# Kernel optimization log

Hardware: AMD Instinct MI355X
Metric: run time of the kernel (lower is better)

The kernel has to match this reference:

```python
import jax, jax.numpy as jnp
import numpy as np

NUM_CLASSES = 43
IMG_SIZE = 640.0
ALPHA, GAMMA = 0.25, 2.0
EPS = 1e-07


def _focal_loss(pred, target):
    p = jnp.clip(pred, EPS, 1.0 - EPS)
    pos = (target > 0.5).astype(p.dtype)
    neg = (target <= 0.5).astype(p.dtype)
    pos_loss = -ALPHA * (1.0 - p) ** GAMMA * jnp.log(p) * pos * target
    neg_loss = -(1.0 - ALPHA) * p ** GAMMA * jnp.log(1.0 - p) * neg * (1.0 - target)
    num_pos = jnp.maximum(pos.sum(), 1.0)
    return (pos_loss + neg_loss).sum() / num_pos


def _generate_targets(bboxes, labels, h, w):
    # bboxes: [B, M, 4] x1y1x2y2 in pixels; labels: [B, M] int (-1 = pad)
    B, M = labels.shape
    stride = IMG_SIZE / h
    x1, y1, x2, y2 = [bboxes[..., i] for i in range(4)]
    cx, cy = (x1 + x2) / 2.0, (y1 + y2) / 2.0
    bw, bh = x2 - x1, y2 - y1
    valid = (labels >= 0) & (bboxes.sum(-1) > 0) & (bw > 0) & (bh > 0)  # [B, M]

    gx = jnp.clip((cx / stride).astype(jnp.int32), 0, w - 1)
    gy = jnp.clip((cy / stride).astype(jnp.int32), 0, h - 1)
    # radius = sqrt(bw*bh)/stride clamped to >=2, then truncated to int
    r = jnp.maximum(jnp.sqrt(bw * bh) / stride, 2.0).astype(jnp.int32).astype(jnp.float32)
    sigma = r / 2.0

    gxf = gx.astype(jnp.float32)[:, :, None, None]  # [B,M,1,1]
    gyf = gy.astype(jnp.float32)[:, :, None, None]
    xg = jnp.arange(w, dtype=jnp.float32)[None, None, None, :]
    yg = jnp.arange(h, dtype=jnp.float32)[None, None, :, None]
    dist_sq = (xg - gxf) ** 2 + (yg - gyf) ** 2  # [B,M,H,W]
    r4 = r[:, :, None, None]
    s4 = sigma[:, :, None, None]
    gauss = jnp.exp(-dist_sq / (2.0 * s4 * s4))
    gauss = gauss * (dist_sq <= (2.0 * r4) ** 2) * valid[:, :, None, None]
    heatmap = gauss.max(axis=1)[:, None]  # [B,1,H,W]; max with implicit 0 init (gauss>=0)

    grid_cx = (gx.astype(jnp.float32) + 0.5) * stride
    grid_cy = (gy.astype(jnp.float32) + 0.5) * stride
    dx = (cx - grid_cx) / stride
    dy = (cy - grid_cy) / stride
    dw = jnp.log(bw / stride + 1e-06)
    dh = jnp.log(bh / stride + 1e-06)

    b_idx = jnp.broadcast_to(jnp.arange(B)[:, None], (B, M))
    gy_s = jnp.where(valid, gy, h)  # out-of-bounds -> dropped
    lab_s = jnp.clip(labels, 0, NUM_CLASSES - 1)

    box_targets = jnp.zeros((B, 4, h, w), jnp.float32)
    box_targets = box_targets.at[b_idx, 0, gy_s, gx].set(dx, mode='drop')
    box_targets = box_targets.at[b_idx, 1, gy_s, gx].set(dy, mode='drop')
    box_targets = box_targets.at[b_idx, 2, gy_s, gx].set(dw, mode='drop')
    box_targets = box_targets.at[b_idx, 3, gy_s, gx].set(dh, mode='drop')
    class_targets = jnp.zeros((B, NUM_CLASSES, h, w), jnp.float32)
    class_targets = class_targets.at[b_idx, lab_s, gy_s, gx].set(1.0, mode='drop')
    mask = jnp.zeros((B, 1, h, w), jnp.float32)
    mask = mask.at[b_idx, 0, gy_s, gx].set(1.0, mode='drop')
    return heatmap, box_targets, class_targets, mask


def setup_inputs() -> dict:
    key = jax.random.key(0)
    k1, k2, k3, k4, k5, k6 = jax.random.split(key, 6)
    B, M, H, W = 16, 64, 160, 160
    pred_heatmap = jax.random.uniform(k1, (B, 1, H, W), jnp.float32)
    pred_boxes = jax.random.normal(k2, (B, 4, H, W), jnp.float32)
    pred_classes = jax.random.normal(k3, (B, NUM_CLASSES, H, W), jnp.float32)
    pts = jax.random.uniform(k4, (B, M, 2, 2), jnp.float32) * IMG_SIZE  # two corners
    lo = jnp.min(pts, axis=2)
    hi = jnp.max(pts, axis=2) + 1.0
    bboxes = jnp.concatenate([lo, hi], axis=-1)  # x1,y1,x2,y2
    labels = jax.random.randint(k5, (B, M), 0, NUM_CLASSES)
    drop = jax.random.uniform(k6, (B, M)) < 0.3
    labels = jnp.where(drop, -1, labels).astype(jnp.int64)
    return {"pred_heatmap": pred_heatmap, "pred_boxes": pred_boxes,
            "pred_classes": pred_classes, "bboxes": bboxes, "labels": labels}


def reference(pred_heatmap, pred_boxes, pred_classes, bboxes, labels):
    B, _, h, w = pred_heatmap.shape
    t_heat, t_box, t_cls, mask = _generate_targets(bboxes, labels, h, w)
    heat_loss = _focal_loss(pred_heatmap, t_heat)
    num_pos = jnp.maximum(mask.sum(), 1.0)
    l1 = jnp.abs(pred_boxes * mask - t_box * mask).sum()
    box_loss = jnp.where(num_pos > 1, l1 / num_pos, 0.0)
    cmask = jnp.broadcast_to(mask, t_cls.shape)
    cls_raw = _focal_loss(jax.nn.sigmoid(pred_classes) * cmask, t_cls * cmask)
    cls_loss = jnp.where(num_pos > 1, cls_raw, 0.0)
    total = heat_loss + box_loss + cls_loss  # lambdas all 1.0
    return total
```

## Files before the change

### kernel.cpp

```cpp
#include <hip/hip_runtime.h>

#define HH 160
#define WW 160
#define HW (HH*WW)
#define NB 16
#define NM 64
#define NC 43
#define BLKX 25
#define NHEAT (NB*BLKX)
#define NCELL (NB*16)

constexpr float STRIDE = 4.0f;
constexpr float EPSF = 1e-7f;
constexpr float BIGF = 3.4e38f;

__device__ __forceinline__ void box_geom4(const float4* __restrict__ bb4,
                                          const int* __restrict__ labels, int t,
                                          bool& valid, int& gx, int& gy,
                                          float& cx, float& cy, float& bw, float& bh) {
  float4 v = bb4[t];
  cx = (v.x + v.z) * 0.5f;
  cy = (v.y + v.w) * 0.5f;
  bw = v.z - v.x;
  bh = v.w - v.y;
  int lab = labels[t];
  valid = (lab >= 0) && ((v.x + v.y + v.z + v.w) > 0.0f) && (bw > 0.0f) && (bh > 0.0f);
  int tgx = (int)(cx * 0.25f);
  int tgy = (int)(cy * 0.25f);
  gx = tgx < 0 ? 0 : (tgx > WW - 1 ? WW - 1 : tgx);
  gy = tgy < 0 ? 0 : (tgy > HH - 1 ? HH - 1 : tgy);
}

__global__ __launch_bounds__(256) void k_fused(const float* __restrict__ pred_heat,
                                               const float* __restrict__ pred_boxes,
                                               const float* __restrict__ pred_classes,
                                               const float4* __restrict__ bboxes,
                                               const int* __restrict__ labels,
                                               float2* __restrict__ heatp,
                                               float4* __restrict__ cellsp) {
  __shared__ float4 sp[NM];
  __shared__ float lred[4];
  __shared__ int nred[4];
  __shared__ float4 cred[4];

  int b = blockIdx.y, bx = blockIdx.x;
  int tid = threadIdx.x;
  int wave = tid >> 6, lane = tid & 63;

  int pixbase = bx * 1024 + tid * 4;
  int idx = b * HW + pixbase;
  float4 pr4 = *(const float4*)(pred_heat + idx);

  bool cellsblk = (bx < 16);
  bool iswin = false;
  float xcls = 0.0f, pbv = 0.0f;
  unsigned long long cm = 0;
  float cx_m, cy_m, bw_m, bh_m;
  int gx_m, gy_m;
  if (cellsblk) {
    int m = bx * 4 + wave;
    int lbox = b * NM + lane;
    bool valid; int gx, gy; float cx, cy, bw, bh;
    box_geom4(bboxes, labels, lbox, valid, gx, gy, cx, cy, bw, bh);
    int lab = labels[lbox]; lab = lab < 0 ? 0 : (lab > NC - 1 ? NC - 1 : lab);

    int valid_m = __shfl((int)valid, m);
    gx_m = __shfl(gx, m); gy_m = __shfl(gy, m);
    cx_m = __shfl(cx, m); cy_m = __shfl(cy, m);
    bw_m = __shfl(bw, m); bh_m = __shfl(bh, m);

    if (valid_m) {
      bool maps = valid && (gx == gx_m) && (gy == gy_m);
      unsigned long long mk = __ballot(maps);
      if ((63 - __clzll(mk)) == m) {
        iswin = true;
        cm = maps ? (1ull << lab) : 0ull;
        #pragma unroll
        for (int o = 1; o < 64; o <<= 1) cm |= __shfl_xor(cm, o);
        int celloff = gy_m * WW + gx_m;
        if (lane < NC)
          xcls = pred_classes[(size_t)b * NC * HW + (size_t)lane * HW + celloff];
        else if (lane < NC + 4)
          pbv = pred_boxes[(size_t)b * 4 * HW + (size_t)(lane - NC) * HW + celloff];
      }
    }
  }

  if (tid < NM) {
    int t = b * NM + tid;
    bool valid; int gx, gy; float cx, cy, bw, bh;
    box_geom4(bboxes, labels, t, valid, gx, gy, cx, cy, bw, bh);
    float rf = fmaxf(sqrtf(bw * bh) * 0.25f, 2.0f);
    float r = (float)(int)rf;
    float z = 2.0f / (r * r);
    float gxf = (float)gx, gyf = (float)gy;
    float4 p;
    p.x = z;
    p.y = -2.0f * z * gxf;
    p.z = -2.0f * z * gyf;
    p.w = valid ? z * fmaf(gxf, gxf, gyf * gyf) : __int_as_float(0x7fc00000);
    sp[tid] = p;
  }
  __syncthreads();

  int row = pixbase / WW;
  float xf0 = (float)(pixbase - row * WW);
  float yf = (float)row;
  float xf1 = xf0 + 1.0f, xf2 = xf0 + 2.0f, xf3 = xf0 + 3.0f;
  float yy = yf * yf;
  float s0 = fmaf(xf0, xf0, yy), s1 = fmaf(xf1, xf1, yy);
  float s2 = fmaf(xf2, xf2, yy), s3 = fmaf(xf3, xf3, yy);

  float m0 = BIGF, m1 = BIGF, m2 = BIGF, m3 = BIGF;
  #pragma unroll
  for (int m = 0; m < NM; m += 2) {
    float4 c0 = sp[m], c1 = sp[m + 1];
    { float base = fmaf(c0.z, yf, c0.w);
      m0 = fminf(m0, fmaf(c0.x, s0, fmaf(c0.y, xf0, base)));
      m1 = fminf(m1, fmaf(c0.x, s1, fmaf(c0.y, xf1, base)));
      m2 = fminf(m2, fmaf(c0.x, s2, fmaf(c0.y, xf2, base)));
      m3 = fminf(m3, fmaf(c0.x, s3, fmaf(c0.y, xf3, base))); }
    { float base = fmaf(c1.z, yf, c1.w);
      m0 = fminf(m0, fmaf(c1.x, s0, fmaf(c1.y, xf0, base)));
      m1 = fminf(m1, fmaf(c1.x, s1, fmaf(c1.y, xf1, base)));
      m2 = fminf(m2, fmaf(c1.x, s2, fmaf(c1.y, xf2, base)));
      m3 = fminf(m3, fmaf(c1.x, s3, fmaf(c1.y, xf3, base))); }
  }

  float t0 = (m0 <= 8.0f) ? __expf(-m0) : 0.0f;
  float t1 = (m1 <= 8.0f) ? __expf(-m1) : 0.0f;
  float t2 = (m2 <= 8.0f) ? __expf(-m2) : 0.0f;
  float t3 = (m3 <= 8.0f) ? __expf(-m3) : 0.0f;
  float p0 = fminf(fmaxf(pr4.x, EPSF), 1.0f - EPSF);
  float p1 = fminf(fmaxf(pr4.y, EPSF), 1.0f - EPSF);
  float p2 = fminf(fmaxf(pr4.z, EPSF), 1.0f - EPSF);
  float p3 = fminf(fmaxf(pr4.w, EPSF), 1.0f - EPSF);
  float q0 = 1.0f - p0, q1 = 1.0f - p1, q2 = 1.0f - p2, q3 = 1.0f - p3;
  bool o0 = t0 > 0.5f, o1 = t1 > 0.5f, o2 = t2 > 0.5f, o3 = t3 > 0.5f;
  float lg0 = __logf(o0 ? p0 : q0), lg1 = __logf(o1 ? p1 : q1);
  float lg2 = __logf(o2 ? p2 : q2), lg3 = __logf(o3 ? p3 : q3);
  float cf0 = o0 ? (-0.25f * q0 * q0 * t0) : (-0.75f * p0 * p0 * (1.0f - t0));
  float cf1 = o1 ? (-0.25f * q1 * q1 * t1) : (-0.75f * p1 * p1 * (1.0f - t1));
  float cf2 = o2 ? (-0.25f * q2 * q2 * t2) : (-0.75f * p2 * p2 * (1.0f - t2));
  float cf3 = o3 ? (-0.25f * q3 * q3 * t3) : (-0.75f * p3 * p3 * (1.0f - t3));
  float loss = fmaf(cf0, lg0, cf1 * lg1) + fmaf(cf2, lg2, cf3 * lg3);

  int cnt = __popcll(__ballot(o0)) + __popcll(__ballot(o1)) +
            __popcll(__ballot(o2)) + __popcll(__ballot(o3));
  #pragma unroll
  for (int off = 32; off > 0; off >>= 1) loss += __shfl_down(loss, off);
  if (lane == 0) { lred[wave] = loss; nred[wave] = cnt; }
  __syncthreads();
  if (tid == 0)
    heatp[b * BLKX + bx] = make_float2(lred[0] + lred[1] + lred[2] + lred[3],
                                       (float)(nred[0] + nred[1] + nred[2] + nred[3]));

  if (cellsblk) {
    float l1 = 0.0f, csum = 0.0f, cnt1 = 0.0f, npos = 0.0f;
    if (iswin) {
      if (lane < NC) {
        float s = 1.0f / (1.0f + __expf(-xcls));
        float pc = fminf(fmaxf(s, EPSF), 1.0f - EPSF);
        float omc = 1.0f - pc;
        csum = ((cm >> lane) & 1ull) ? (-0.25f * omc * omc * __logf(pc))
                                     : (-0.75f * pc * pc * __logf(omc));
      }
      float dxv = (cx_m - ((float)gx_m + 0.5f) * STRIDE) * 0.25f;
      float dyv = (cy_m - ((float)gy_m + 0.5f) * STRIDE) * 0.25f;
      int li = lane - NC;
      float tlin = (li == 0) ? dxv : dyv;
      float tlog = __logf(((li == 2) ? bw_m : bh_m) * 0.25f + 1e-6f);
      float targ = (li < 2) ? tlin : tlog;
      float l1c = (li >= 0 && li < 4) ? fabsf(pbv - targ) : 0.0f;
      #pragma unroll
      for (int o = 32; o > 0; o >>= 1) {
        csum += __shfl_down(csum, o);
        l1c  += __shfl_down(l1c, o);
      }
      l1 = l1c;
      cnt1 = (lane == 0) ? 1.0f : 0.0f;
      npos = (float)__popcll(cm);
    }
    if (lane == 0) cred[wave] = make_float4(l1, cnt1, csum, npos);
    __syncthreads();
    if (tid == 0) {
      float4 a = cred[0], c1 = cred[1], c2 = cred[2], c3 = cred[3];
      cellsp[b * 16 + bx] = make_float4(a.x + c1.x + c2.x + c3.x,
                                        a.y + c1.y + c2.y + c3.y,
                                        a.z + c1.z + c2.z + c3.z,
                                        a.w + c1.w + c2.w + c3.w);
    }
  }
}

__global__ __launch_bounds__(512) void k_final(const float2* __restrict__ heatp,
                                               const float4* __restrict__ cellsp,
                                               float* __restrict__ out) {
  int t = threadIdx.x;
  double hs = 0.0, hc = 0.0, l1 = 0.0, mc = 0.0, cs = 0.0, cp = 0.0;
  if (t < NHEAT) {
    float2 v = heatp[t];
    hs = (double)v.x; hc = (double)v.y;
  }
  if (t < NCELL) {
    float4 e = cellsp[t];
    l1 = (double)e.x; mc = (double)e.y; cs = (double)e.z; cp = (double)e.w;
  }
  #pragma unroll
  for (int off = 32; off > 0; off >>= 1) {
    hs += __shfl_down(hs, off); hc += __shfl_down(hc, off);
    l1 += __shfl_down(l1, off); mc += __shfl_down(mc, off);
    cs += __shfl_down(cs, off); cp += __shfl_down(cp, off);
  }
  __shared__ double fin[8][6];
  int wave = t >> 6;
  if ((t & 63) == 0) {
    fin[wave][0] = hs; fin[wave][1] = hc; fin[wave][2] = l1;
    fin[wave][3] = mc; fin[wave][4] = cs; fin[wave][5] = cp;
  }
  __syncthreads();
  if (t == 0) {
    double HS = 0, HC = 0, L1 = 0, MC = 0, CS = 0, CP = 0;
    #pragma unroll
    for (int i = 0; i < 8; ++i) {
      HS += fin[i][0]; HC += fin[i][1]; L1 += fin[i][2];
      MC += fin[i][3]; CS += fin[i][4]; CP += fin[i][5];
    }
    double nph = HC < 1.0 ? 1.0 : HC;
    float heat = (float)(HS / nph);
    float box = 0.0f, cls = 0.0f;
    if (MC > 1.5) {
      box = (float)(L1 / MC);
      double c = CP < 1.0 ? 1.0 : CP;
      cls = (float)(CS / c);
    }
    out[0] = heat + box + cls;
  }
}

extern "C" void kernel_launch(void* const* d_in, const int* in_sizes, int n_in,
                              void* d_out, int out_size, void* d_ws, size_t ws_size,
                              hipStream_t stream) {
  const float*  pred_heat    = (const float*)d_in[0];
  const float*  pred_boxes   = (const float*)d_in[1];
  const float*  pred_classes = (const float*)d_in[2];
  const float4* bboxes       = (const float4*)d_in[3];
  const int*    labels       = (const int*)d_in[4];

  char* ws = (char*)d_ws;
  float2* heatp  = (float2*)ws;
  float4* cellsp = (float4*)(ws + 3200);

  dim3 grid(BLKX, NB);
  k_fused<<<grid, 256, 0, stream>>>(pred_heat, pred_boxes, pred_classes,
                                    bboxes, labels, heatp, cellsp);
  k_final<<<1, 512, 0, stream>>>(heatp, cellsp, (float*)d_out);
}
```

Baseline: 14.45 us.

## Split heatmap and per-cell work into separate block groups

The per-box cell work (class focal loss and box L1 at winning cells) now runs in 16 extra blocks per batch instead of sharing blocks with the heatmap computation. This is meant to shorten the critical path of the first 16 blocks, which previously did both jobs serially, and to spread the gathers across more CUs. The cost is 256 more blocks in the grid, each with its own launch and reduction overhead.

After: 14.43 us. No clear change (-0.1%).

```diff
diff --git a/kernel.cpp b/kernel.cpp
--- a/kernel.cpp
+++ b/kernel.cpp
@@ -47,145 +47,138 @@
   int tid = threadIdx.x;
   int wave = tid >> 6, lane = tid & 63;
 
-  int pixbase = bx * 1024 + tid * 4;
-  int idx = b * HW + pixbase;
-  float4 pr4 = *(const float4*)(pred_heat + idx);
-
-  bool cellsblk = (bx < 16);
-  bool iswin = false;
-  float xcls = 0.0f, pbv = 0.0f;
-  unsigned long long cm = 0;
-  float cx_m, cy_m, bw_m, bh_m;
-  int gx_m, gy_m;
-  if (cellsblk) {
-    int m = bx * 4 + wave;
+  if (bx < BLKX) {
+    int pixbase = bx * 1024 + tid * 4;
+    int idx = b * HW + pixbase;
+    float4 pr4 = *(const float4*)(pred_heat + idx);
+
+    if (tid < NM) {
+      int t = b * NM + tid;
+      bool valid; int gx, gy; float cx, cy, bw, bh;
+      box_geom4(bboxes, labels, t, valid, gx, gy, cx, cy, bw, bh);
+      float rf = fmaxf(sqrtf(bw * bh) * 0.25f, 2.0f);
+      float r = (float)(int)rf;
+      float z = 2.0f / (r * r);
+      float gxf = (float)gx, gyf = (float)gy;
+      float4 p;
+      p.x = z;
+      p.y = -2.0f * z * gxf;
+      p.z = -2.0f * z * gyf;
+      p.w = valid ? z * fmaf(gxf, gxf, gyf * gyf) : __int_as_float(0x7fc00000);
+      sp[tid] = p;
+    }
+    __syncthreads();
+
+    int row = pixbase / WW;
+    float xf0 = (float)(pixbase - row * WW);
+    float yf = (float)row;
+    float xf1 = xf0 + 1.0f, xf2 = xf0 + 2.0f, xf3 = xf0 + 3.0f;
+    float yy = yf * yf;
+    float s0 = fmaf(xf0, xf0, yy), s1 = fmaf(xf1, xf1, yy);
+    float s2 = fmaf(xf2, xf2, yy), s3 = fmaf(xf3, xf3, yy);
+
+    float m0 = BIGF, m1 = BIGF, m2 = BIGF, m3 = BIGF;
+    #pragma unroll
+    for (int m = 0; m < NM; m += 2) {
+      float4 c0 = sp[m], c1 = sp[m + 1];
+      { float base = fmaf(c0.z, yf, c0.w);
+        m0 = fminf(m0, fmaf(c0.x, s0, fmaf(c0.y, xf0, base)));
+        m1 = fminf(m1, fmaf(c0.x, s1, fmaf(c0.y, xf1, base)));
+        m2 = fminf(m2, fmaf(c0.x, s2, fmaf(c0.y, xf2, base)));
+        m3 = fminf(m3, fmaf(c0.x, s3, fmaf(c0.y, xf3, base))); }
+      { float base = fmaf(c1.z, yf, c1.w);
+        m0 = fminf(m0, fmaf(c1.x, s0, fmaf(c1.y, xf0, base)));
+        m1 = fminf(m1, fmaf(c1.x, s1, fmaf(c1.y, xf1, base)));
+        m2 = fminf(m2, fmaf(c1.x, s2, fmaf(c1.y, xf2, base)));
+        m3 = fminf(m3, fmaf(c1.x, s3, fmaf(c1.y, xf3, base))); }
+    }
+
+    float t0 = (m0 <= 8.0f) ? __expf(-m0) : 0.0f;
+    float t1 = (m1 <= 8.0f) ? __expf(-m1) : 0.0f;
+    float t2 = (m2 <= 8.0f) ? __expf(-m2) : 0.0f;
+    float t3 = (m3 <= 8.0f) ? __expf(-m3) : 0.0f;
+    float p0 = fminf(fmaxf(pr4.x, EPSF), 1.0f - EPSF);
+    float p1 = fminf(fmaxf(pr4.y, EPSF), 1.0f - EPSF);
+    float p2 = fminf(fmaxf(pr4.z, EPSF), 1.0f - EPSF);
+    float p3 = fminf(fmaxf(pr4.w, EPSF), 1.0f - EPSF);
+    float q0 = 1.0f - p0, q1 = 1.0f - p1, q2 = 1.0f - p2, q3 = 1.0f - p3;
+    bool o0 = t0 > 0.5f, o1 = t1 > 0.5f, o2 = t2 > 0.5f, o3 = t3 > 0.5f;
+    float lg0 = __logf(o0 ? p0 : q0), lg1 = __logf(o1 ? p1 : q1);
+    float lg2 = __logf(o2 ? p2 : q2), lg3 = __logf(o3 ? p3 : q3);
+    float cf0 = o0 ? (-0.25f * q0 * q0 * t0) : (-0.75f * p0 * p0 * (1.0f - t0));
+    float cf1 = o1 ? (-0.25f * q1 * q1 * t1) : (-0.75f * p1 * p1 * (1.0f - t1));
+    float cf2 = o2 ? (-0.25f * q2 * q2 * t2) : (-0.75f * p2 * p2 * (1.0f - t2));
+    float cf3 = o3 ? (-0.25f * q3 * q3 * t3) : (-0.75f * p3 * p3 * (1.0f - t3));
+    float loss = fmaf(cf0, lg0, cf1 * lg1) + fmaf(cf2, lg2, cf3 * lg3);
+
+    int cnt = __popcll(__ballot(o0)) + __popcll(__ballot(o1)) +
+              __popcll(__ballot(o2)) + __popcll(__ballot(o3));
+    #pragma unroll
+    for (int off = 32; off > 0; off >>= 1) loss += __shfl_down(loss, off);
+    if (lane == 0) { lred[wave] = loss; nred[wave] = cnt; }
+    __syncthreads();
+    if (tid == 0)
+      heatp[b * BLKX + bx] =
+          make_float2(lred[0] + lred[1] + lred[2] + lred[3],
+                      (float)(nred[0] + nred[1] + nred[2] + nred[3]));
+  } else {
+    int cb = bx - BLKX;
+    int m = cb * 4 + wave;
     int lbox = b * NM + lane;
     bool valid; int gx, gy; float cx, cy, bw, bh;
     box_geom4(bboxes, labels, lbox, valid, gx, gy, cx, cy, bw, bh);
     int lab = labels[lbox]; lab = lab < 0 ? 0 : (lab > NC - 1 ? NC - 1 : lab);
 
-    int valid_m = __shfl((int)valid, m);
-    gx_m = __shfl(gx, m); gy_m = __shfl(gy, m);
-    cx_m = __shfl(cx, m); cy_m = __shfl(cy, m);
-    bw_m = __shfl(bw, m); bh_m = __shfl(bh, m);
-
+    int   valid_m = __shfl((int)valid, m);
+    int   gx_m = __shfl(gx, m), gy_m = __shfl(gy, m);
+    float cx_m = __shfl(cx, m), cy_m = __shfl(cy, m);
+    float bw_m = __shfl(bw, m), bh_m = __shfl(bh, m);
+
+    float l1 = 0.0f, csum = 0.0f, cnt1 = 0.0f, npos = 0.0f;
     if (valid_m) {
       bool maps = valid && (gx == gx_m) && (gy == gy_m);
       unsigned long long mk = __ballot(maps);
       if ((63 - __clzll(mk)) == m) {
-        iswin = true;
-        cm = maps ? (1ull << lab) : 0ull;
+        unsigned long long cm = maps ? (1ull << lab) : 0ull;
         #pragma unroll
         for (int o = 1; o < 64; o <<= 1) cm |= __shfl_xor(cm, o);
         int celloff = gy_m * WW + gx_m;
+
+        float xcls = 0.0f, pbv = 0.0f;
         if (lane < NC)
           xcls = pred_classes[(size_t)b * NC * HW + (size_t)lane * HW + celloff];
         else if (lane < NC + 4)
           pbv = pred_boxes[(size_t)b * 4 * HW + (size_t)(lane - NC) * HW + celloff];
+
+        if (lane < NC) {
+          float s = 1.0f / (1.0f + __expf(-xcls));
+          float pc = fminf(fmaxf(s, EPSF), 1.0f - EPSF);
+          float omc = 1.0f - pc;
+          csum = ((cm >> lane) & 1ull) ? (-0.25f * omc * omc * __logf(pc))
+                                       : (-0.75f * pc * pc * __logf(omc));
+        }
+        float dxv = (cx_m - ((float)gx_m + 0.5f) * STRIDE) * 0.25f;
+        float dyv = (cy_m - ((float)gy_m + 0.5f) * STRIDE) * 0.25f;
+        int li = lane - NC;
+        float tlin = (li == 0) ? dxv : dyv;
+        float tlog = __logf(((li == 2) ? bw_m : bh_m) * 0.25f + 1e-6f);
+        float targ = (li < 2) ? tlin : tlog;
+        float l1c = (li >= 0 && li < 4) ? fabsf(pbv - targ) : 0.0f;
+        #pragma unroll
+        for (int o = 32; o > 0; o >>= 1) {
+          csum += __shfl_down(csum, o);
+          l1c  += __shfl_down(l1c, o);
+        }
+        l1 = l1c;
+        cnt1 = (lane == 0) ? 1.0f : 0.0f;
+        npos = (float)__popcll(cm);
       }
-    }
-  }
-
-  if (tid < NM) {
-    int t = b * NM + tid;
-    bool valid; int gx, gy; float cx, cy, bw, bh;
-    box_geom4(bboxes, labels, t, valid, gx, gy, cx, cy, bw, bh);
-    float rf = fmaxf(sqrtf(bw * bh) * 0.25f, 2.0f);
-    float r = (float)(int)rf;
-    float z = 2.0f / (r * r);
-    float gxf = (float)gx, gyf = (float)gy;
-    float4 p;
-    p.x = z;
-    p.y = -2.0f * z * gxf;
-    p.z = -2.0f * z * gyf;
-    p.w = valid ? z * fmaf(gxf, gxf, gyf * gyf) : __int_as_float(0x7fc00000);
-    sp[tid] = p;
-  }
-  __syncthreads();
-
-  int row = pixbase / WW;
-  float xf0 = (float)(pixbase - row * WW);
-  float yf = (float)row;
-  float xf1 = xf0 + 1.0f, xf2 = xf0 + 2.0f, xf3 = xf0 + 3.0f;
-  float yy = yf * yf;
-  float s0 = fmaf(xf0, xf0, yy), s1 = fmaf(xf1, xf1, yy);
-  float s2 = fmaf(xf2, xf2, yy), s3 = fmaf(xf3, xf3, yy);
-
-  float m0 = BIGF, m1 = BIGF, m2 = BIGF, m3 = BIGF;
-  #pragma unroll
-  for (int m = 0; m < NM; m += 2) {
-    float4 c0 = sp[m], c1 = sp[m + 1];
-    { float base = fmaf(c0.z, yf, c0.w);
-      m0 = fminf(m0, fmaf(c0.x, s0, fmaf(c0.y, xf0, base)));
-      m1 = fminf(m1, fmaf(c0.x, s1, fmaf(c0.y, xf1, base)));
-      m2 = fminf(m2, fmaf(c0.x, s2, fmaf(c0.y, xf2, base)));
-      m3 = fminf(m3, fmaf(c0.x, s3, fmaf(c0.y, xf3, base))); }
-    { float base = fmaf(c1.z, yf, c1.w);
-      m0 = fminf(m0, fmaf(c1.x, s0, fmaf(c1.y, xf0, base)));
-      m1 = fminf(m1, fmaf(c1.x, s1, fmaf(c1.y, xf1, base)));
-      m2 = fminf(m2, fmaf(c1.x, s2, fmaf(c1.y, xf2, base)));
-      m3 = fminf(m3, fmaf(c1.x, s3, fmaf(c1.y, xf3, base))); }
-  }
-
-  float t0 = (m0 <= 8.0f) ? __expf(-m0) : 0.0f;
-  float t1 = (m1 <= 8.0f) ? __expf(-m1) : 0.0f;
-  float t2 = (m2 <= 8.0f) ? __expf(-m2) : 0.0f;
-  float t3 = (m3 <= 8.0f) ? __expf(-m3) : 0.0f;
-  float p0 = fminf(fmaxf(pr4.x, EPSF), 1.0f - EPSF);
-  float p1 = fminf(fmaxf(pr4.y, EPSF), 1.0f - EPSF);
-  float p2 = fminf(fmaxf(pr4.z, EPSF), 1.0f - EPSF);
-  float p3 = fminf(fmaxf(pr4.w, EPSF), 1.0f - EPSF);
-  float q0 = 1.0f - p0, q1 = 1.0f - p1, q2 = 1.0f - p2, q3 = 1.0f - p3;
-  bool o0 = t0 > 0.5f, o1 = t1 > 0.5f, o2 = t2 > 0.5f, o3 = t3 > 0.5f;
-  float lg0 = __logf(o0 ? p0 : q0), lg1 = __logf(o1 ? p1 : q1);
-  float lg2 = __logf(o2 ? p2 : q2), lg3 = __logf(o3 ? p3 : q3);
-  float cf0 = o0 ? (-0.25f * q0 * q0 * t0) : (-0.75f * p0 * p0 * (1.0f - t0));
-  float cf1 = o1 ? (-0.25f * q1 * q1 * t1) : (-0.75f * p1 * p1 * (1.0f - t1));
-  float cf2 = o2 ? (-0.25f * q2 * q2 * t2) : (-0.75f * p2 * p2 * (1.0f - t2));
-  float cf3 = o3 ? (-0.25f * q3 * q3 * t3) : (-0.75f * p3 * p3 * (1.0f - t3));
-  float loss = fmaf(cf0, lg0, cf1 * lg1) + fmaf(cf2, lg2, cf3 * lg3);
-
-  int cnt = __popcll(__ballot(o0)) + __popcll(__ballot(o1)) +
-            __popcll(__ballot(o2)) + __popcll(__ballot(o3));
-  #pragma unroll
-  for (int off = 32; off > 0; off >>= 1) loss += __shfl_down(loss, off);
-  if (lane == 0) { lred[wave] = loss; nred[wave] = cnt; }
-  __syncthreads();
-  if (tid == 0)
-    heatp[b * BLKX + bx] = make_float2(lred[0] + lred[1] + lred[2] + lred[3],
-                                       (float)(nred[0] + nred[1] + nred[2] + nred[3]));
-
-  if (cellsblk) {
-    float l1 = 0.0f, csum = 0.0f, cnt1 = 0.0f, npos = 0.0f;
-    if (iswin) {
-      if (lane < NC) {
-        float s = 1.0f / (1.0f + __expf(-xcls));
-        float pc = fminf(fmaxf(s, EPSF), 1.0f - EPSF);
-        float omc = 1.0f - pc;
-        csum = ((cm >> lane) & 1ull) ? (-0.25f * omc * omc * __logf(pc))
-                                     : (-0.75f * pc * pc * __logf(omc));
-      }
-      float dxv = (cx_m - ((float)gx_m + 0.5f) * STRIDE) * 0.25f;
-      float dyv = (cy_m - ((float)gy_m + 0.5f) * STRIDE) * 0.25f;
-      int li = lane - NC;
-      float tlin = (li == 0) ? dxv : dyv;
-      float tlog = __logf(((li == 2) ? bw_m : bh_m) * 0.25f + 1e-6f);
-      float targ = (li < 2) ? tlin : tlog;
-      float l1c = (li >= 0 && li < 4) ? fabsf(pbv - targ) : 0.0f;
-      #pragma unroll
-      for (int o = 32; o > 0; o >>= 1) {
-        csum += __shfl_down(csum, o);
-        l1c  += __shfl_down(l1c, o);
-      }
-      l1 = l1c;
-      cnt1 = (lane == 0) ? 1.0f : 0.0f;
-      npos = (float)__popcll(cm);
     }
     if (lane == 0) cred[wave] = make_float4(l1, cnt1, csum, npos);
     __syncthreads();
     if (tid == 0) {
       float4 a = cred[0], c1 = cred[1], c2 = cred[2], c3 = cred[3];
-      cellsp[b * 16 + bx] = make_float4(a.x + c1.x + c2.x + c3.x,
+      cellsp[b * 16 + cb] = make_float4(a.x + c1.x + c2.x + c3.x,
                                         a.y + c1.y + c2.y + c3.y,
                                         a.z + c1.z + c2.z + c3.z,
                                         a.w + c1.w + c2.w + c3.w);
@@ -251,7 +244,7 @@
   float2* heatp  = (float2*)ws;
   float4* cellsp = (float4*)(ws + 3200);
 
-  dim3 grid(BLKX, NB);
+  dim3 grid(BLKX + 16, NB);
   k_fused<<<grid, 256, 0, stream>>>(pred_heat, pred_boxes, pred_classes,
                                     bboxes, labels, heatp, cellsp);
   k_final<<<1, 512, 0, stream>>>(heatp, cellsp, (float*)d_out);
```
